# Performance work log

Hardware: AMD Instinct MI355X
Metric: run time of the kernel (lower is better)

## Reference

```python
import jax, jax.numpy as jnp
import numpy as np

ALPHA = 0.2  # LeakyReLU negative slope
NEG_INF = -9e15


def setup_inputs() -> dict:
    key = jax.random.key(0)
    k1, k2, k3, k4 = jax.random.split(key, 4)
    B, N, F_in, F_out = 8, 2048, 256, 128
    x = jax.random.normal(k1, (B, N, F_in), dtype=jnp.float32)
    adj = jax.random.randint(k2, (B, N, N), 0, 2, dtype=jnp.int32)
    # xavier-uniform-like init
    limW = float(np.sqrt(6.0 / (F_in + F_out)))
    W = jax.random.uniform(k3, (F_in, F_out), jnp.float32, -limW, limW)
    lima = float(np.sqrt(6.0 / (2 * F_out + 1)))
    a = jax.random.uniform(k4, (2 * F_out, 1), jnp.float32, -lima, lima)
    return {"x": x, "adj": adj, "W": W, "a": a}


def reference(x, adj, W, a):
    # x: [B, N, F_in], adj: [B, N, N], W: [F_in, F_out], a: [2*F_out, 1]
    F_out = W.shape[1]
    h = jnp.einsum('bnf,fo->bno', x, W)            # [B, N, F_out]
    a1 = a[:F_out, 0]                               # attends to source node i
    a2 = a[F_out:, 0]                               # attends to target node j
    f1 = h @ a1                                     # [B, N]
    f2 = h @ a2                                     # [B, N]
    # e[b,i,j] = leakyrelu(a1.h_i + a2.h_j) -- factored form of the concat trick
    e = jax.nn.leaky_relu(f1[:, :, None] + f2[:, None, :], negative_slope=ALPHA)
    attention = jnp.where(adj > 0, e, NEG_INF)
    attention = jax.nn.softmax(attention, axis=2)   # [B, N, N]
    # dropout is identity in eval mode
    h_prime = jnp.einsum('bij,bjo->bio', attention, h)  # [B, N, F_out]
    return jax.nn.elu(h_prime)                      # concat=True -> ELU
```

## Files before the change

### kernel.cpp

```cpp
#include <hip/hip_runtime.h>
#include <stdint.h>

#define BB   8
#define NN   2048
#define FIN  256
#define FOUT 128

using short8 = __attribute__((ext_vector_type(8))) short;
using f32x4  = __attribute__((ext_vector_type(4))) float;

__device__ __forceinline__ unsigned short rbf(float f) {
    return (unsigned short)((__float_as_uint(f) + 0x8000u) >> 16);
}

__device__ __forceinline__ void mfma_calib(int m, int quad, int* Mlab, int* Nlab) {
    short8 pa1, pb1, pa2, pb2;
    const short one = (short)0x3F80;
    const short mb  = (short)rbf((float)m);
#pragma unroll
    for (int j = 0; j < 8; ++j) { pa1[j] = 0; pa2[j] = 0; pb1[j] = mb; pb2[j] = one; }
    if (quad == 0) { pa1[0] = one; pa2[0] = mb; }
    f32x4 zz = {0.f, 0.f, 0.f, 0.f};
    f32x4 c1 = __builtin_amdgcn_mfma_f32_16x16x32_bf16(pa1, pb1, zz, 0, 0, 0);
    f32x4 c2 = __builtin_amdgcn_mfma_f32_16x16x32_bf16(pa2, pb2, zz, 0, 0, 0);
#pragma unroll
    for (int r = 0; r < 4; ++r) {
        Nlab[r] = ((int)c1[r]) & 15;
        Mlab[r] = ((int)c2[r]) & 15;
    }
}

__global__ __launch_bounds__(256) void gat_wt(const float* __restrict__ W,
                                              unsigned short* __restrict__ wt) {
    const int g  = blockIdx.x * 256 + threadIdx.x;
    const int k  = g >> 5;
    const int o4 = (g & 31) << 2;
    float4 wv = *(const float4*)(W + (k << 7) + o4);
    wt[((o4 + 0) << 8) + k] = rbf(wv.x);
    wt[((o4 + 1) << 8) + k] = rbf(wv.y);
    wt[((o4 + 2) << 8) + k] = rbf(wv.z);
    wt[((o4 + 3) << 8) + k] = rbf(wv.w);
}

__global__ __launch_bounds__(256) void gat_h3(
        const float* __restrict__ x, const unsigned short* __restrict__ wt,
        const float* __restrict__ a, unsigned short* __restrict__ ht,
        float* __restrict__ f1, float* __restrict__ f2) {
    __shared__ unsigned short xs[16][264];
    __shared__ float hs[16][132];
    const int bk   = blockIdx.x;
    const int R0   = bk << 4;
    const int b    = R0 >> 11;
    const int il0  = R0 & (NN - 1);
    const int tid  = threadIdx.x;
    const int w    = tid >> 6;
    const int lane = tid & 63;
    const int m    = lane & 15;
    const int quad = lane >> 4;

#pragma unroll
    for (int rr = 0; rr < 4; ++rr) {
        const int row = (w << 2) + rr;
        float4 xv = *(const float4*)(x + (size_t)(R0 + row) * FIN + (lane << 2));
        ushort4 c4;
        c4.x = rbf(xv.x); c4.y = rbf(xv.y); c4.z = rbf(xv.z); c4.w = rbf(xv.w);
        *(ushort4*)(&xs[row][lane << 2]) = c4;
    }
    int Mlab[4], Nlab[4];
    mfma_calib(m, quad, Mlab, Nlab);
    __syncthreads();

    f32x4 zz = {0.f, 0.f, 0.f, 0.f};
    f32x4 acc[2] = {zz, zz};
#pragma unroll
    for (int kc = 0; kc < 8; ++kc) {
        const int k0 = (kc << 5) + (quad << 3);
        short8 av = *(const short8*)(&xs[m][k0]);
#pragma unroll
        for (int t = 0; t < 2; ++t) {
            const int ot = (w << 1) + t;
            short8 bw = *(const short8*)(wt + (((ot << 4) + m) << 8) + k0);
            acc[t] = __builtin_amdgcn_mfma_f32_16x16x32_bf16(av, bw, acc[t], 0, 0, 0);
        }
    }
#pragma unroll
    for (int t = 0; t < 2; ++t)
#pragma unroll
        for (int r = 0; r < 4; ++r)
            hs[Mlab[r]][(((w << 1) + t) << 4) + Nlab[r]] = acc[t][r];
    __syncthreads();

    {
        const int i   = tid >> 4;
        const int seg = tid & 15;
        const int o0  = seg << 3;
        float s1 = 0.f, s2 = 0.f;
#pragma unroll
        for (int e = 0; e < 8; ++e) {
            float hv = hs[i][o0 + e];
            s1 = fmaf(hv, a[o0 + e], s1);
            s2 = fmaf(hv, a[FOUT + o0 + e], s2);
        }
        s1 += __shfl_xor(s1, 1); s1 += __shfl_xor(s1, 2);
        s1 += __shfl_xor(s1, 4); s1 += __shfl_xor(s1, 8);
        s2 += __shfl_xor(s2, 1); s2 += __shfl_xor(s2, 2);
        s2 += __shfl_xor(s2, 4); s2 += __shfl_xor(s2, 8);
        if (seg == 0) { f1[R0 + i] = s1; f2[R0 + i] = s2; }
    }
    {
        const int o  = tid >> 1;
        const int i8 = (tid & 1) << 3;
        short8 hv;
#pragma unroll
        for (int e = 0; e < 8; ++e) hv[e] = (short)rbf(hs[i8 + e][o]);
        *(short8*)(ht + ((size_t)((b << 7) + o) << 11) + il0 + i8) = hv;
    }
}

__global__ __launch_bounds__(256, 4) void gat_s16(
        const int* __restrict__ adj, const unsigned short* __restrict__ ht,
        const float* __restrict__ f1, const float* __restrict__ f2,
        float* __restrict__ out) {
    const int bk   = blockIdx.x;
    const int b    = bk & 7;
    const int i0   = (bk >> 3) << 4;
    const int tid  = threadIdx.x;
    const int w    = tid >> 6;
    const int lane = tid & 63;
    const int m    = lane & 15;
    const int quad = lane >> 4;

    __shared__ float accb[4][16][130];
    __shared__ float sbuf[4][16];

    const int gi0 = (b << 11) + i0;
    const float f1a = f1[gi0 + m];
    const int* adjr0 = adj + ((size_t)(gi0 + m) << 11);
    const float* f2b = f2 + (b << 11);
    const unsigned short* htb = ht + ((size_t)b << 18);

    f32x4 zz = {0.f, 0.f, 0.f, 0.f};
    f32x4 acc[8];
#pragma unroll
    for (int t = 0; t < 8; ++t) acc[t] = zz;
    float s1 = 0.f;

    const int jb = (w << 9) + (quad << 3);
#pragma unroll 2
    for (int c = 0; c < 16; ++c) {
        const int j0 = jb + (c << 5);
        short8 hf[8];
#pragma unroll
        for (int ot = 0; ot < 8; ++ot)
            hf[ot] = *(const short8*)(htb + ((size_t)((ot << 4) + m) << 11) + j0);

        int4   aA0 = *(const int4*)(adjr0 + j0);
        int4   aA1 = *(const int4*)(adjr0 + j0 + 4);
        float4 fa  = *(const float4*)(f2b + j0);
        float4 fb  = *(const float4*)(f2b + j0 + 4);
        float fm[8] = {fa.x, fa.y, fa.z, fa.w, fb.x, fb.y, fb.z, fb.w};

        float pA[8];
        {
            int am[8] = {aA0.x, aA0.y, aA0.z, aA0.w, aA1.x, aA1.y, aA1.z, aA1.w};
#pragma unroll
            for (int u = 0; u < 8; ++u) {
                float e = f1a + fm[u];
                pA[u] = (am[u] > 0) ? __expf(fmaxf(e, 0.2f * e)) : 0.f;
            }
        }
        s1 += ((pA[0] + pA[1]) + (pA[2] + pA[3])) + ((pA[4] + pA[5]) + (pA[6] + pA[7]));

        short8 pf1;
#pragma unroll
        for (int u = 0; u < 8; ++u) pf1[u] = (short)rbf(pA[u]);

#pragma unroll
        for (int ot = 0; ot < 8; ++ot)
            acc[ot] = __builtin_amdgcn_mfma_f32_16x16x32_bf16(pf1, hf[ot], acc[ot], 0, 0, 0);
    }

    s1 += __shfl_xor(s1, 16); s1 += __shfl_xor(s1, 32);
    if (lane < 16) sbuf[w][lane] = s1;

    int Mlab[4], Nlab[4];
    mfma_calib(m, quad, Mlab, Nlab);

#pragma unroll
    for (int ot = 0; ot < 8; ++ot)
#pragma unroll
        for (int r = 0; r < 4; ++r)
            accb[w][Mlab[r]][(ot << 4) + Nlab[r]] = acc[ot][r];
    __syncthreads();

    {
        const int row = tid >> 4;
        const int o0  = (tid & 15) << 3;
        const float s = (sbuf[0][row] + sbuf[1][row]) + (sbuf[2][row] + sbuf[3][row]);
        const float inv = 1.0f / s;
        float* orow = out + (((size_t)gi0 + row) << 7) + o0;
#pragma unroll
        for (int v4 = 0; v4 < 2; ++v4) {
            float4 rv;
            float y;
            const int oo = o0 + (v4 << 2);
            y = (accb[0][row][oo + 0] + accb[1][row][oo + 0] + accb[2][row][oo + 0] + accb[3][row][oo + 0]) * inv;
            rv.x = y > 0.f ? y : expm1f(y);
            y = (accb[0][row][oo + 1] + accb[1][row][oo + 1] + accb[2][row][oo + 1] + accb[3][row][oo + 1]) * inv;
            rv.y = y > 0.f ? y : expm1f(y);
            y = (accb[0][row][oo + 2] + accb[1][row][oo + 2] + accb[2][row][oo + 2] + accb[3][row][oo + 2]) * inv;
            rv.z = y > 0.f ? y : expm1f(y);
            y = (accb[0][row][oo + 3] + accb[1][row][oo + 3] + accb[2][row][oo + 3] + accb[3][row][oo + 3]) * inv;
            rv.w = y > 0.f ? y : expm1f(y);
            *(float4*)(orow + (v4 << 2)) = rv;
        }
    }
}

extern "C" void kernel_launch(void* const* d_in, const int* in_sizes, int n_in,
                              void* d_out, int out_size, void* d_ws, size_t ws_size,
                              hipStream_t stream) {
    const float* x   = nullptr;
    const int*   adj = nullptr;
    const float* W   = nullptr;
    const float* a   = nullptr;
    for (int i = 0; i < n_in; ++i) {
        const long s = in_sizes[i];
        if      (s == (long)BB * NN * NN)  adj = (const int*)d_in[i];
        else if (s == (long)BB * NN * FIN) x   = (const float*)d_in[i];
        else if (s == (long)FIN * FOUT)    W   = (const float*)d_in[i];
        else if (s == 2L * FOUT)           a   = (const float*)d_in[i];
    }
    if (!x)   x   = (const float*)d_in[0];
    if (!adj) adj = (const int*)d_in[1];
    if (!W)   W   = (const float*)d_in[2];
    if (!a)   a   = (const float*)d_in[3];
    float* out = (float*)d_out;

    unsigned short* wt = (unsigned short*)d_ws;
    unsigned short* ht = wt + 32768;
    float* f1 = (float*)(ht + (size_t)BB * NN * FOUT);
    float* f2 = f1 + BB * NN;

    hipLaunchKernelGGL(gat_wt,  dim3(32),   dim3(256), 0, stream, W, wt);
    hipLaunchKernelGGL(gat_h3,  dim3(1024), dim3(256), 0, stream, x, wt, a, ht, f1, f2);
    hipLaunchKernelGGL(gat_s16, dim3(1024), dim3(256), 0, stream, adj, ht, f1, f2, out);
}
```

Baseline: 277.0 us.

## Pack adjacency into a tiled bitmask and retile ht for coalesced MFMA loads

Adds a streaming pre-pass that turns the int32 adjacency matrix into a 1-byte-per-8-neighbours bitmask, stored in the exact order the attention kernel consumes it. The producer of ht now writes it tiled by wave, chunk and output tile, so each lane's short8 B-fragment load is contiguous across the wave instead of strided across 2048-element rows. The attention kernel reads one byte of mask per iteration instead of two int4 adjacency loads. This removes heavy strided gather traffic from the main loop, at the cost of an extra kernel launch that still reads all of adj and writes a small mask buffer.

Result: faster. 245.7 us (-11.3%).

```diff
diff --git a/kernel.cpp b/kernel.cpp
--- a/kernel.cpp
+++ b/kernel.cpp
@@ -42,7 +42,27 @@
     wt[((o4 + 3) << 8) + k] = rbf(wv.w);
 }
 
-__global__ __launch_bounds__(256) void gat_h3(
+__global__ __launch_bounds__(256) void gat_bm2(const int* __restrict__ adj,
+                                               unsigned char* __restrict__ bm) {
+    const int row = blockIdx.x;
+    const int tid = threadIdx.x;
+    const int4* p = (const int4*)(adj + ((size_t)row << 11) + (tid << 3));
+    int4 a0 = p[0];
+    int4 a1 = p[1];
+    unsigned int b = (unsigned int)(a0.x > 0)
+                   | ((unsigned int)(a0.y > 0) << 1)
+                   | ((unsigned int)(a0.z > 0) << 2)
+                   | ((unsigned int)(a0.w > 0) << 3)
+                   | ((unsigned int)(a1.x > 0) << 4)
+                   | ((unsigned int)(a1.y > 0) << 5)
+                   | ((unsigned int)(a1.z > 0) << 6)
+                   | ((unsigned int)(a1.w > 0) << 7);
+    const int w = tid >> 6, c = (tid >> 2) & 15, q = tid & 3;
+    bm[((size_t)(row >> 5) << 13) + (c << 9) + (w << 7) + (q << 5) + (row & 31)]
+        = (unsigned char)b;
+}
+
+__global__ __launch_bounds__(256) void gat_h4(
         const float* __restrict__ x, const unsigned short* __restrict__ wt,
         const float* __restrict__ a, unsigned short* __restrict__ ht,
         float* __restrict__ f1, float* __restrict__ f2) {
@@ -110,15 +130,21 @@
     {
         const int o  = tid >> 1;
         const int i8 = (tid & 1) << 3;
+        const int jj = il0 + i8;
+        const int wj = jj >> 9;
+        const int cj = (jj >> 5) & 15;
+        const int qj = (jj >> 3) & 3;
         short8 hv;
 #pragma unroll
         for (int e = 0; e < 8; ++e) hv[e] = (short)rbf(hs[i8 + e][o]);
-        *(short8*)(ht + ((size_t)((b << 7) + o) << 11) + il0 + i8) = hv;
-    }
-}
-
-__global__ __launch_bounds__(256, 4) void gat_s16(
-        const int* __restrict__ adj, const unsigned short* __restrict__ ht,
+        const size_t addr = ((size_t)b << 18) + ((size_t)wj << 16) + (cj << 12)
+                          + ((o >> 4) << 9) + (((qj << 4) + (o & 15)) << 3);
+        *(short8*)(ht + addr) = hv;
+    }
+}
+
+__global__ __launch_bounds__(256, 4) void gat_s1f(
+        const unsigned char* __restrict__ bm, const unsigned short* __restrict__ ht,
         const float* __restrict__ f1, const float* __restrict__ f2,
         float* __restrict__ out) {
     const int bk   = blockIdx.x;
@@ -135,9 +161,11 @@
 
     const int gi0 = (b << 11) + i0;
     const float f1a = f1[gi0 + m];
-    const int* adjr0 = adj + ((size_t)(gi0 + m) << 11);
+    const unsigned char* bmb = bm + (((size_t)gi0 >> 5) << 13);
+    const int mq = (w << 7) + (quad << 5) + (i0 & 16) + m;
     const float* f2b = f2 + (b << 11);
-    const unsigned short* htb = ht + ((size_t)b << 18);
+    const unsigned short* htb = ht + ((size_t)b << 18) + ((size_t)w << 16);
+    const int jb  = (w << 9) + (quad << 3);
 
     f32x4 zz = {0.f, 0.f, 0.f, 0.f};
     f32x4 acc[8];
@@ -145,29 +173,25 @@
     for (int t = 0; t < 8; ++t) acc[t] = zz;
     float s1 = 0.f;
 
-    const int jb = (w << 9) + (quad << 3);
 #pragma unroll 2
     for (int c = 0; c < 16; ++c) {
+        short8 hf[8];
+        const unsigned short* hp = htb + (c << 12);
+#pragma unroll
+        for (int ot = 0; ot < 8; ++ot)
+            hf[ot] = *(const short8*)(hp + (ot << 9) + (lane << 3));
+
+        const unsigned int mA = bmb[(c << 9) + mq];
         const int j0 = jb + (c << 5);
-        short8 hf[8];
-#pragma unroll
-        for (int ot = 0; ot < 8; ++ot)
-            hf[ot] = *(const short8*)(htb + ((size_t)((ot << 4) + m) << 11) + j0);
-
-        int4   aA0 = *(const int4*)(adjr0 + j0);
-        int4   aA1 = *(const int4*)(adjr0 + j0 + 4);
-        float4 fa  = *(const float4*)(f2b + j0);
-        float4 fb  = *(const float4*)(f2b + j0 + 4);
+        float4 fa = *(const float4*)(f2b + j0);
+        float4 fb = *(const float4*)(f2b + j0 + 4);
         float fm[8] = {fa.x, fa.y, fa.z, fa.w, fb.x, fb.y, fb.z, fb.w};
 
         float pA[8];
-        {
-            int am[8] = {aA0.x, aA0.y, aA0.z, aA0.w, aA1.x, aA1.y, aA1.z, aA1.w};
-#pragma unroll
-            for (int u = 0; u < 8; ++u) {
-                float e = f1a + fm[u];
-                pA[u] = (am[u] > 0) ? __expf(fmaxf(e, 0.2f * e)) : 0.f;
-            }
+#pragma unroll
+        for (int u = 0; u < 8; ++u) {
+            float e = f1a + fm[u];
+            pA[u] = (mA & (1u << u)) ? __expf(fmaxf(e, 0.2f * e)) : 0.f;
         }
         s1 += ((pA[0] + pA[1]) + (pA[2] + pA[3])) + ((pA[4] + pA[5]) + (pA[6] + pA[7]));
 
@@ -239,10 +263,12 @@
 
     unsigned short* wt = (unsigned short*)d_ws;
     unsigned short* ht = wt + 32768;
-    float* f1 = (float*)(ht + (size_t)BB * NN * FOUT);
-    float* f2 = f1 + BB * NN;
-
-    hipLaunchKernelGGL(gat_wt,  dim3(32),   dim3(256), 0, stream, W, wt);
-    hipLaunchKernelGGL(gat_h3,  dim3(1024), dim3(256), 0, stream, x, wt, a, ht, f1, f2);
-    hipLaunchKernelGGL(gat_s16, dim3(1024), dim3(256), 0, stream, adj, ht, f1, f2, out);
-}
+    float* f1  = (float*)(ht + (size_t)BB * NN * FOUT);
+    float* f2  = f1 + BB * NN;
+    unsigned char* bmw = (unsigned char*)(f2 + BB * NN);
+
+    hipLaunchKernelGGL(gat_wt,  dim3(32),    dim3(256), 0, stream, W, wt);
+    hipLaunchKernelGGL(gat_bm2, dim3(16384), dim3(256), 0, stream, adj, bmw);
+    hipLaunchKernelGGL(gat_h4,  dim3(1024),  dim3(256), 0, stream, x, wt, a, ht, f1, f2);
+    hipLaunchKernelGGL(gat_s1f, dim3(1024),  dim3(256), 0, stream, bmw, ht, f1, f2, out);
+}
```
